# Performance work log

Measured on AMD Instinct MI355X. Metric: run time of the kernel, lower is better.

Reference implementation:

```python
import jax, jax.numpy as jnp
import numpy as np

N = 50000      # num nodes
E = 800000     # num edges
D = 128        # hidden_dim
H = 2          # num_heads
A = H * D      # all_head_size


def setup_inputs() -> dict:
    key = jax.random.key(0)
    ks = jax.random.split(key, 18)
    rn = lambda k, shape, s=1.0: jax.random.normal(k, shape, jnp.float32) * s
    w = 0.05  # small init scale for weights (glorot-ish)
    return {
        "x_0": rn(ks[0], (N, D)),
        "x_1": rn(ks[1], (N, D)),
        "edge_attr": rn(ks[2], (E, D)),
        "edges": jax.random.randint(ks[3], (2, E), 0, N, jnp.int64 if jax.config.jax_enable_x64 else jnp.int32),
        "edge_types": jax.random.randint(ks[4], (E,), 0, 8, jnp.int64 if jax.config.jax_enable_x64 else jnp.int32),
        # Attention projections (stored [in, out]; equals torch Linear y = x @ W)
        "Wq": rn(ks[5], (D, A), w),   "bq": jnp.zeros((A,), jnp.float32),
        "Wk": rn(ks[6], (2 * D, A), w), "bk": jnp.zeros((A,), jnp.float32),
        "Wv": rn(ks[7], (2 * D, A), w), "bv": jnp.zeros((A,), jnp.float32),
        "Wo": rn(ks[8], (A, D), w),   "bo": jnp.zeros((D,), jnp.float32),
        # GRUCell params: gates ordered (r, z, n) as in torch
        "W_ih": rn(ks[9], (D, 3 * D), w),  "b_ih": rn(ks[10], (3 * D,), w),
        "W_hh": rn(ks[11], (D, 3 * D), w), "b_hh": rn(ks[12], (3 * D,), w),
    }


def _gru_cell(x, h, W_ih, b_ih, W_hh, b_hh):
    gi = x @ W_ih + b_ih
    gh = h @ W_hh + b_hh
    i_r, i_z, i_n = jnp.split(gi, 3, axis=-1)
    h_r, h_z, h_n = jnp.split(gh, 3, axis=-1)
    r = jax.nn.sigmoid(i_r + h_r)
    z = jax.nn.sigmoid(i_z + h_z)
    n = jnp.tanh(i_n + r * h_n)
    return (1.0 - z) * n + z * h


def reference(x_0, x_1, edge_attr, edges, edge_types,
              Wq, bq, Wk, bk, Wv, bv, Wo, bo, W_ih, b_ih, W_hh, b_hh):
    src, dst = edges[0], edges[1]            # x_j <- src, x_i <- dst
    q = (x_0[dst] @ Wq + bq).reshape(-1, H, D)            # [E,H,D]
    kv_in = jnp.concatenate([edge_attr, x_1[src]], -1)    # [E,2D]
    k = (kv_in @ Wk + bk).reshape(-1, H, D)
    v = (kv_in @ Wv + bv).reshape(-1, H, D)
    alpha = jnp.sum(q * k, -1) / jnp.sqrt(jnp.float32(D)) # [E,H]
    alpha = jax.nn.leaky_relu(alpha, 0.2)
    # segment softmax over dst (PyG softmax semantics, eps = 1e-16)
    m = jax.ops.segment_max(alpha, dst, num_segments=N)
    e = jnp.exp(alpha - m[dst])
    denom = jax.ops.segment_sum(e, dst, num_segments=N)
    a = e / (denom[dst] + 1e-16)                           # [E,H]
    aggr = jax.ops.segment_sum(a[:, :, None] * v, dst, num_segments=N)  # [N,H,D]
    msg = aggr.reshape(N, A) @ Wo + bo                     # [N,D]
    # GRUCell(input=x_0, hidden=attn_message); target_idxes = all nodes
    return _gru_cell(x_0, msg, W_ih, b_ih, W_hh, b_hh)
```

## Files before the change

kernel.cpp:

```cpp
#include <hip/hip_runtime.h>
#include <hip/hip_bf16.h>
#include <math.h>

#define NN 50000
#define EE 800000
#define MPAD 50048

#define OFF_QQBF   0ull
#define OFF_KVBF   12900000ull
#define OFF_AGGBF  25900000ull
#define OFF_MSGBF  45300000ull
#define OFF_INT    48600000ull
#define OFF_WCATQ  50500000ull
#define OFF_WCATKV 50600000ull
#define OFF_WBIG   50700000ull
#define OFF_WGRU   50800000ull
#define OFF_BCATQ  51000000ull
#define OFF_BCATKV 51001000ull
#define OFF_BGRU   51002000ull
#define OFF_BO2    51003000ull
#define OFF_PQ     51010000ull
#define OFF_PKV    51050000ull
#define OFF_PBIG   51090000ull
#define OFF_PGRU   51130000ull
#define OFF_X0BF   51200000ull

typedef short bf16x8 __attribute__((ext_vector_type(8)));
typedef float f32x4 __attribute__((ext_vector_type(4)));
typedef float fv4 __attribute__((ext_vector_type(4)));

__device__ inline unsigned short f2bf(float f) {
  unsigned u = __float_as_uint(f);
  return (unsigned short)((u + 0x7FFFu + ((u >> 16) & 1u)) >> 16);
}
__device__ inline float bf2f(unsigned short u) {
  return __uint_as_float((unsigned)u << 16);
}
__device__ inline float4 bf2f4(ushort4 u) {
  float4 r;
  r.x = bf2f(u.x); r.y = bf2f(u.y); r.z = bf2f(u.z); r.w = bf2f(u.w);
  return r;
}

__global__ void prep_all(const float* __restrict__ Wq, const float* __restrict__ bq,
                         const float* __restrict__ Wk, const float* __restrict__ bk,
                         const float* __restrict__ Wv, const float* __restrict__ bv,
                         const float* __restrict__ Wo, const float* __restrict__ bo,
                         const float* __restrict__ W_ih, const float* __restrict__ b_ih,
                         const float* __restrict__ W_hh, const float* __restrict__ b_hh,
                         float* __restrict__ WcatQ, float* __restrict__ bcatQ,
                         float* __restrict__ WcatKV, float* __restrict__ bcatKV,
                         float* __restrict__ Wbig, float* __restrict__ WgruCat,
                         float* __restrict__ bgru, float* __restrict__ bo2,
                         int* __restrict__ zint) {
  const int bid = blockIdx.x, j = threadIdx.x;
  if (bid < 129) {
    int c0 = bid, h = j >> 7, c = j & 127;
    const float* wkrow = Wk + (size_t)c * 256 + h * 128;
    float acc = 0.f;
    if (c0 < 128) {
      const float* wqrow = Wq + (size_t)c0 * 256 + h * 128;
      for (int d = 0; d < 128; d++) acc += wqrow[d] * wkrow[d];
      WcatQ[c0 * 512 + 256 + j] = acc;
    } else {
      for (int d = 0; d < 128; d++) acc += bq[h * 128 + d] * wkrow[d];
      bcatQ[256 + j] = acc;
    }
  } else if (bid < 257) {
    int r = bid - 129;
    WcatQ[r * 512 + j] = Wq[r * 256 + j];
    if (j < 256) WcatKV[r * 256 + j] = Wk[(size_t)(128 + r) * 256 + j];
    if (r == 0) {
      bcatQ[j] = bq[j];
      if (j < 256) bcatKV[j] = bk[j];
    }
  } else if (bid < 513) {
    int r = (bid - 257) * 2 + (j >> 7), jj = j & 127;
    int h = (r >> 7) & 1, c = r & 127;
    int srow = (r < 256) ? c : 128 + c;
    float acc = 0.f;
    for (int d = 0; d < 128; d++)
      acc += Wv[(size_t)srow * 256 + h * 128 + d] * Wo[(size_t)(h * 128 + d) * 128 + jj];
    Wbig[r * 128 + jj] = acc;
  } else if (bid < 769) {
    int r = bid - 513;
    for (int c = j; c < 512; c += 256) {
      float v;
      if (r < 128) v = (c < 384) ? W_ih[(size_t)r * 384 + c] : 0.f;
      else {
        int rm = r - 128;
        v = (c < 256) ? W_hh[(size_t)rm * 384 + c]
                      : (c < 384 ? 0.f : W_hh[(size_t)rm * 384 + 256 + (c - 384)]);
      }
      WgruCat[(size_t)r * 512 + c] = v;
    }
  } else if (bid == 769) {
    bgru[j] = b_ih[j] + b_hh[j];
    int c1 = j + 256;
    bgru[c1] = (c1 < 384) ? b_ih[c1] : b_hh[c1 - 128];
  } else if (bid == 770) {
    if (j < 128) {
      float acc = bo[j];
      for (int t = 0; t < 256; t++) acc += bv[t] * Wo[(size_t)t * 128 + j];
      bo2[j] = acc;
    }
  } else {
    int g = ((bid - 771) * 256 + j) * 4;
    if (g < 2 * NN) *reinterpret_cast<int4*>(zint + g) = make_int4(0, 0, 0, 0);
  }
}

__global__ __launch_bounds__(1024) void pack_hist(
    const float* __restrict__ WcatQ, const float* __restrict__ WcatKV,
    const float* __restrict__ Wbig, const float* __restrict__ WgruCat,
    unsigned short* __restrict__ pQ, unsigned short* __restrict__ pKV,
    unsigned short* __restrict__ pBig, unsigned short* __restrict__ pGRU,
    const int* __restrict__ edges, int* __restrict__ cnt) {
  const int bid = blockIdx.x, tid = threadIdx.x;
  if (bid < 36) {
    int idx = bid * 1024 + tid;
    const float* W; unsigned short* P; int Nc;
    if (idx < 8192)       { W = WcatQ;   P = pQ;   Nc = 512; }
    else if (idx < 12288) { W = WcatKV;  P = pKV;  Nc = 256; idx -= 8192; }
    else if (idx < 20480) { W = Wbig;    P = pBig; Nc = 128; idx -= 12288; }
    else                  { W = WgruCat; P = pGRU; Nc = 512; idx -= 20480; }
    int nbs = Nc >> 4;
    int lane = idx & 63;
    int pair = idx >> 6;
    int kb = pair / nbs, nb = pair - kb * nbs;
    int kbase = kb * 32 + (lane >> 4) * 8;
    int col = nb * 16 + (lane & 15);
    unsigned short o[8];
#pragma unroll
    for (int j = 0; j < 8; ++j) o[j] = f2bf(W[(size_t)(kbase + j) * Nc + col]);
    *reinterpret_cast<bf16x8*>(P + (size_t)idx * 8) = *reinterpret_cast<bf16x8*>(o);
  } else {
    int e = (bid - 36) * 1024 + tid;
    if (e < EE) atomicAdd(&cnt[edges[EE + e]], 1);
  }
}

__global__ __launch_bounds__(1024) void scan_partial(const int* __restrict__ cnt,
                                                     int* __restrict__ basep,
                                                     int* __restrict__ bsum) {
  __shared__ int sd[1024];
  int t = threadIdx.x, g = blockIdx.x * 1024 + t;
  int v = (g < NN) ? cnt[g] : 0;
  sd[t] = v;
  __syncthreads();
  for (int d = 1; d < 1024; d <<= 1) {
    int add = (t >= d) ? sd[t - d] : 0;
    __syncthreads();
    sd[t] += add;
    __syncthreads();
  }
  if (g < NN) basep[g] = sd[t] - v;
  if (t == 1023) bsum[blockIdx.x] = sd[1023];
}

__global__ __launch_bounds__(1024) void scan_final(const int* __restrict__ bsum,
                                                   const int* __restrict__ basep,
                                                   int* __restrict__ base) {
  __shared__ int s_off;
  const int bid = blockIdx.x, tid = threadIdx.x;
  if (tid < 64) {
    int v = (tid < 49) ? bsum[tid] : 0;
    int incl = v;
#pragma unroll
    for (int off = 1; off < 64; off <<= 1) {
      int o = __shfl_up(incl, off);
      if (tid >= off) incl += o;
    }
    int ex = (bid == 0) ? 0 : __shfl(incl, bid - 1);
    if (tid == 0) s_off = ex;
  }
  __syncthreads();
  int g = bid * 1024 + tid;
  if (g < NN) base[g] = basep[g] + s_off;
  if (bid == 48 && tid == 0) base[NN] = EE;
}

template <int OUT, int AF32, int NF, int EMITA>
__device__ __forceinline__ void gemm_body(
    int bx, int by, const void* __restrict__ Av, const unsigned short* __restrict__ Wp,
    const float* __restrict__ bias, float* __restrict__ C,
    unsigned short* __restrict__ Cbf, unsigned short* __restrict__ Abf,
    int M, int Arows, int K, int Nc, int ldc) {
  const int wid = threadIdx.x >> 6, lane = threadIdx.x & 63;
  const int m0 = by * 64 + wid * 16;
  const int nb0 = bx * NF;
  const int nbs = Nc >> 4;
  const int row = m0 + (lane & 15);
  const int arow = min(row, Arows - 1);
  const int kq = lane >> 4;
  f32x4 acc[NF];
#pragma unroll
  for (int nf = 0; nf < NF; ++nf) acc[nf] = 0.f;
  const int nkb = K >> 5;
  for (int kb = 0; kb < nkb; ++kb) {
    bf16x8 a;
    if (AF32) {
      const float* ap = (const float*)Av + (size_t)arow * K + kb * 32 + kq * 8;
      const float4 f0 = *(const float4*)ap;
      const float4 f1 = *(const float4*)(ap + 4);
      unsigned short t[8] = {f2bf(f0.x), f2bf(f0.y), f2bf(f0.z), f2bf(f0.w),
                             f2bf(f1.x), f2bf(f1.y), f2bf(f1.z), f2bf(f1.w)};
      a = *reinterpret_cast<bf16x8*>(t);
      if (EMITA == 1) {
        if (bx == 0)
          *reinterpret_cast<bf16x8*>(Abf + (size_t)arow * K + kb * 32 + kq * 8) = a;
      } else if (EMITA == 2) {
        if (bx == 0)
          *reinterpret_cast<bf16x8*>(Abf + (size_t)arow * 384 + 256 +
                                     kb * 32 + kq * 8) = a;
      }
    } else {
      a = *reinterpret_cast<const bf16x8*>(
          (const unsigned short*)Av + (size_t)arow * K + kb * 32 + kq * 8);
    }
#pragma unroll
    for (int nf = 0; nf < NF; ++nf) {
      bf16x8 b = *reinterpret_cast<const bf16x8*>(
          Wp + ((size_t)(kb * nbs + nb0 + nf) * 64 + lane) * 8);
      acc[nf] = __builtin_amdgcn_mfma_f32_16x16x32_bf16(a, b, acc[nf], 0, 0, 0);
    }
  }
  const int crow0 = m0 + (lane >> 4) * 4;
  const int ccol = lane & 15;
#pragma unroll
  for (int nf = 0; nf < NF; ++nf) {
    const float bv = bias[(nb0 + nf) * 16 + ccol];
#pragma unroll
    for (int r = 0; r < 4; ++r) {
      float v = acc[nf][r] + bv;
      float vp = __shfl_xor(v, 1);
      const int rr = crow0 + r;
      if (rr < M) {
        if (OUT == 2)
          C[(size_t)rr * ldc + (nb0 + nf) * 16 + ccol] = v;
        if (!(lane & 1)) {
          ushort2 o;
          o.x = f2bf(v);
          o.y = f2bf(vp);
          *reinterpret_cast<ushort2*>(Cbf + (size_t)rr * ldc +
                                      (nb0 + nf) * 16 + (ccol & ~1)) = o;
        }
      }
    }
  }
}

template <int OUT, int AF32, int NF, int EMITA>
__global__ __launch_bounds__(256) void gemm_mfma(
    const void* __restrict__ Av, const unsigned short* __restrict__ Wp,
    const float* __restrict__ bias, float* __restrict__ C,
    unsigned short* __restrict__ Cbf, unsigned short* __restrict__ Abf,
    int M, int Arows, int K, int Nc, int ldc) {
  gemm_body<OUT, AF32, NF, EMITA>(blockIdx.x, blockIdx.y, Av, Wp, bias, C, Cbf,
                                  Abf, M, Arows, K, Nc, ldc);
}

__global__ __launch_bounds__(256) void scatter_proj(
    const int* __restrict__ edges, const int* __restrict__ base,
    int* __restrict__ cursor, int2* __restrict__ epairs,
    const float* __restrict__ x0, const float* __restrict__ x1,
    const unsigned short* __restrict__ pQ, const unsigned short* __restrict__ pKV,
    const float* __restrict__ bcatQ, const float* __restrict__ bcatKV,
    unsigned short* __restrict__ QQbf, unsigned short* __restrict__ KVbf,
    unsigned short* __restrict__ x0bf) {
  const int bid = blockIdx.x;
  if (bid < 3125) {
    int e = bid * 256 + threadIdx.x;
    int s = edges[e];
    int d = edges[EE + e];
    int pos = base[d] + atomicAdd(&cursor[d], 1);
    epairs[pos] = make_int2(e, s);
  } else if (bid < 6253) {
    int pb = bid - 3125;
    gemm_body<1, 1, 8, 1>(pb & 3, pb >> 2, x0, pQ, bcatQ, nullptr, QQbf, x0bf,
                          NN, NN, 128, 512, 512);
  } else {
    int pb = bid - 6253;
    gemm_body<1, 1, 8, 2>(pb & 1, pb >> 1, x1, pKV, bcatKV, nullptr, KVbf, KVbf,
                          NN, NN, 128, 256, 384);
  }
}

__global__ __launch_bounds__(256) void attn_wave_kernel(
    const float* __restrict__ edge_attr, const unsigned short* __restrict__ QQbf,
    const unsigned short* __restrict__ KVbf, const int* __restrict__ base,
    const int2* __restrict__ epairs, unsigned short* __restrict__ aggbf) {
  const int wid = threadIdx.x >> 6, lane = threadIdx.x & 63;
  const int n = blockIdx.x * 4 + wid;
  if (n >= NN) return;
  const int hh = lane >> 5;
  const int l = lane & 31;
  const unsigned short* qp = QQbf + (size_t)n * 512 + 4 * l;
  const float4 q0 = bf2f4(*(const ushort4*)(qp));
  const float4 q1 = bf2f4(*(const ushort4*)(qp + 128));
  const float4 w0 = bf2f4(*(const ushort4*)(qp + 256));
  const float4 w1 = bf2f4(*(const ushort4*)(qp + 384));
  const int beg = base[n], end = base[n + 1];
  float s0 = 0.f, s1 = 0.f;
  float4 ae0 = {0.f, 0.f, 0.f, 0.f}, ae1 = {0.f, 0.f, 0.f, 0.f};
  float4 av0 = {0.f, 0.f, 0.f, 0.f}, av1 = {0.f, 0.f, 0.f, 0.f};
  const float SC = 0.08838834764831845f;
  for (int p = beg; p < end; p += 2) {
    const int pe = min(p + hh, end - 1);
    const bool act = (p + hh < end);
    const int2 es = epairs[pe];
    const fv4 eav = __builtin_nontemporal_load(
        (const fv4*)(edge_attr + (size_t)es.x * 128 + 4 * l));
    const float4 ea = {eav.x, eav.y, eav.z, eav.w};
    const unsigned short* kp = KVbf + (size_t)es.y * 384 + 4 * l;
    const float4 k0 = bf2f4(*(const ushort4*)(kp));
    const float4 k1 = bf2f4(*(const ushort4*)(kp + 128));
    const float4 xb = bf2f4(*(const ushort4*)(kp + 256));
    float p0 = ea.x * w0.x + ea.y * w0.y + ea.z * w0.z + ea.w * w0.w
             + q0.x * k0.x + q0.y * k0.y + q0.z * k0.z + q0.w * k0.w;
    float p1 = ea.x * w1.x + ea.y * w1.y + ea.z * w1.z + ea.w * w1.w
             + q1.x * k1.x + q1.y * k1.y + q1.z * k1.z + q1.w * k1.w;
#pragma unroll
    for (int off = 16; off; off >>= 1) {
      p0 += __shfl_xor(p0, off);
      p1 += __shfl_xor(p1, off);
    }
    float a0 = p0 * SC; a0 = (a0 < 0.f) ? 0.2f * a0 : a0;
    float a1 = p1 * SC; a1 = (a1 < 0.f) ? 0.2f * a1 : a1;
    const float x0 = act ? __expf(a0) : 0.f;
    const float x1 = act ? __expf(a1) : 0.f;
    s0 += x0; s1 += x1;
    ae0.x += x0 * ea.x; ae0.y += x0 * ea.y; ae0.z += x0 * ea.z; ae0.w += x0 * ea.w;
    ae1.x += x1 * ea.x; ae1.y += x1 * ea.y; ae1.z += x1 * ea.z; ae1.w += x1 * ea.w;
    av0.x += x0 * xb.x; av0.y += x0 * xb.y; av0.z += x0 * xb.z; av0.w += x0 * xb.w;
    av1.x += x1 * xb.x; av1.y += x1 * xb.y; av1.z += x1 * xb.z; av1.w += x1 * xb.w;
  }
  s0 += __shfl_xor(s0, 32); s1 += __shfl_xor(s1, 32);
  ae0.x += __shfl_xor(ae0.x, 32); ae0.y += __shfl_xor(ae0.y, 32);
  ae0.z += __shfl_xor(ae0.z, 32); ae0.w += __shfl_xor(ae0.w, 32);
  ae1.x += __shfl_xor(ae1.x, 32); ae1.y += __shfl_xor(ae1.y, 32);
  ae1.z += __shfl_xor(ae1.z, 32); ae1.w += __shfl_xor(ae1.w, 32);
  av0.x += __shfl_xor(av0.x, 32); av0.y += __shfl_xor(av0.y, 32);
  av0.z += __shfl_xor(av0.z, 32); av0.w += __shfl_xor(av0.w, 32);
  av1.x += __shfl_xor(av1.x, 32); av1.y += __shfl_xor(av1.y, 32);
  av1.z += __shfl_xor(av1.z, 32); av1.w += __shfl_xor(av1.w, 32);
  const float i0 = 1.f / (s0 + 1e-16f), i1 = 1.f / (s1 + 1e-16f);
  if (hh == 0) {
    unsigned short* op = aggbf + (size_t)n * 512 + 4 * l;
    ushort4 o;
    o.x = f2bf(ae0.x * i0); o.y = f2bf(ae0.y * i0);
    o.z = f2bf(ae0.z * i0); o.w = f2bf(ae0.w * i0);
    *(ushort4*)op = o;
    o.x = f2bf(ae1.x * i1); o.y = f2bf(ae1.y * i1);
    o.z = f2bf(ae1.z * i1); o.w = f2bf(ae1.w * i1);
    *(ushort4*)(op + 128) = o;
    o.x = f2bf(av0.x * i0); o.y = f2bf(av0.y * i0);
    o.z = f2bf(av0.z * i0); o.w = f2bf(av0.w * i0);
    *(ushort4*)(op + 256) = o;
    o.x = f2bf(av1.x * i1); o.y = f2bf(av1.y * i1);
    o.z = f2bf(av1.z * i1); o.w = f2bf(av1.w * i1);
    *(ushort4*)(op + 384) = o;
  }
}

__global__ __launch_bounds__(256) void gru_fused(
    const unsigned short* __restrict__ x0bf, const unsigned short* __restrict__ msgbf,
    const unsigned short* __restrict__ pGRU, const float* __restrict__ bgru,
    float* __restrict__ out) {
  const int wid = threadIdx.x >> 6, lane = threadIdx.x & 63;
  const int m0 = blockIdx.y * 64 + wid * 16;
  const int xq = blockIdx.x;
  const int row = m0 + (lane & 15);
  const int ar = min(row, NN - 1);
  const int kq = lane >> 4;
  f32x4 acc[4][2];
#pragma unroll
  for (int g = 0; g < 4; ++g)
#pragma unroll
    for (int f = 0; f < 2; ++f) acc[g][f] = 0.f;
  for (int kb = 0; kb < 8; ++kb) {
    bf16x8 a;
    if (kb < 4) {
      a = *reinterpret_cast<const bf16x8*>(x0bf + (size_t)ar * 128 +
                                           kb * 32 + kq * 8);
    } else {
      a = *reinterpret_cast<const bf16x8*>(msgbf + (size_t)ar * 128 +
                                           (kb - 4) * 32 + kq * 8);
    }
#pragma unroll
    for (int g = 0; g < 4; ++g)
#pragma unroll
      for (int f = 0; f < 2; ++f) {
        const int nf = g * 8 + xq * 2 + f;
        bf16x8 b = *reinterpret_cast<const bf16x8*>(
            pGRU + ((size_t)(kb * 32 + nf) * 64 + lane) * 8);
        acc[g][f] = __builtin_amdgcn_mfma_f32_16x16x32_bf16(a, b, acc[g][f], 0, 0, 0);
      }
  }
  const int crow0 = m0 + (lane >> 4) * 4;
  const int ccol = lane & 15;
#pragma unroll
  for (int f = 0; f < 2; ++f) {
    const int d = xq * 32 + f * 16 + ccol;
    const float brs = bgru[d], bzs = bgru[128 + d];
    const float bin = bgru[256 + d], bhn = bgru[384 + d];
#pragma unroll
    for (int r = 0; r < 4; ++r) {
      const int rr = crow0 + r;
      if (rr < NN) {
        const float rs = acc[0][f][r] + brs;
        const float zs = acc[1][f][r] + bzs;
        const float iv = acc[2][f][r] + bin;
        const float hv = acc[3][f][r] + bhn;
        const float rg = 1.f / (1.f + __expf(-rs));
        const float zg = 1.f / (1.f + __expf(-zs));
        const float ng = tanhf(iv + rg * hv);
        const float h = bf2f(msgbf[(size_t)rr * 128 + d]);
        out[(size_t)rr * 128 + d] = (1.f - zg) * ng + zg * h;
      }
    }
  }
}

extern "C" void kernel_launch(void* const* d_in, const int* in_sizes, int n_in,
                              void* d_out, int out_size, void* d_ws, size_t ws_size,
                              hipStream_t stream) {
  const float* x0 = (const float*)d_in[0];
  const float* x1 = (const float*)d_in[1];
  const float* edge_attr = (const float*)d_in[2];
  const int* edges = (const int*)d_in[3];
  const float* Wq = (const float*)d_in[5];
  const float* bq = (const float*)d_in[6];
  const float* Wk = (const float*)d_in[7];
  const float* bk = (const float*)d_in[8];
  const float* Wv = (const float*)d_in[9];
  const float* bv = (const float*)d_in[10];
  const float* Wo = (const float*)d_in[11];
  const float* bo = (const float*)d_in[12];
  const float* W_ih = (const float*)d_in[13];
  const float* b_ih = (const float*)d_in[14];
  const float* W_hh = (const float*)d_in[15];
  const float* b_hh = (const float*)d_in[16];
  float* out = (float*)d_out;
  float* wsf = (float*)d_ws;

  unsigned short* QQbf  = (unsigned short*)(wsf + OFF_QQBF);
  unsigned short* KVbf  = (unsigned short*)(wsf + OFF_KVBF);
  unsigned short* aggbf = (unsigned short*)(wsf + OFF_AGGBF);
  unsigned short* msgbf = (unsigned short*)(wsf + OFF_MSGBF);
  unsigned short* x0bf  = (unsigned short*)(wsf + OFF_X0BF);
  int* ip    = (int*)(wsf + OFF_INT);
  int* cntb  = ip;
  int* curb  = ip + NN;
  int* bpart = ip + 2 * NN;
  int* baseb = ip + 3 * NN;
  int* bsumb = ip + 4 * NN + 1;
  int2* epairs = (int2*)(ip + 4 * NN + 130);
  float* WcatQ  = wsf + OFF_WCATQ;
  float* WcatKV = wsf + OFF_WCATKV;
  float* Wbigb  = wsf + OFF_WBIG;
  float* WgruC  = wsf + OFF_WGRU;
  float* bcatQ  = wsf + OFF_BCATQ;
  float* bcatKV = wsf + OFF_BCATKV;
  float* bgru   = wsf + OFF_BGRU;
  float* bo2    = wsf + OFF_BO2;
  unsigned short* pQ   = (unsigned short*)(wsf + OFF_PQ);
  unsigned short* pKV  = (unsigned short*)(wsf + OFF_PKV);
  unsigned short* pBig = (unsigned short*)(wsf + OFF_PBIG);
  unsigned short* pGRU = (unsigned short*)(wsf + OFF_PGRU);

  prep_all<<<871, 256, 0, stream>>>(Wq, bq, Wk, bk, Wv, bv, Wo, bo, W_ih, b_ih,
                                    W_hh, b_hh, WcatQ, bcatQ, WcatKV, bcatKV,
                                    Wbigb, WgruC, bgru, bo2, ip);
  pack_hist<<<818, 1024, 0, stream>>>(WcatQ, WcatKV, Wbigb, WgruC,
                                      pQ, pKV, pBig, pGRU, edges, cntb);
  scan_partial<<<49, 1024, 0, stream>>>(cntb, bpart, bsumb);
  scan_final<<<49, 1024, 0, stream>>>(bsumb, bpart, baseb);
  scatter_proj<<<7817, 256, 0, stream>>>(edges, baseb, curb, epairs,
                                         x0, x1, pQ, pKV, bcatQ, bcatKV,
                                         QQbf, KVbf, x0bf);
  attn_wave_kernel<<<(NN + 3) / 4, 256, 0, stream>>>(edge_attr, QQbf, KVbf,
                                                     baseb, epairs, aggbf);
  gemm_mfma<1, 0, 4, 0><<<dim3(2, MPAD / 64), 256, 0, stream>>>(
      aggbf, pBig, bo2, nullptr, msgbf, nullptr, NN, NN, 512, 128, 128);
  gru_fused<<<dim3(4, MPAD / 64), 256, 0, stream>>>(x0bf, msgbf, pGRU, bgru, out);
}
```

Measured before the change: 397.4 us.

## Fold Wk x1-part into per-node query weights, gather raw bf16 x1

```diff
diff --git a/kernel.cpp b/kernel.cpp
--- a/kernel.cpp
+++ b/kernel.cpp
@@ -7,23 +7,22 @@
 #define MPAD 50048
 
 #define OFF_QQBF   0ull
-#define OFF_KVBF   12900000ull
-#define OFF_AGGBF  25900000ull
-#define OFF_MSGBF  45300000ull
-#define OFF_INT    48600000ull
-#define OFF_WCATQ  50500000ull
-#define OFF_WCATKV 50600000ull
-#define OFF_WBIG   50700000ull
-#define OFF_WGRU   50800000ull
-#define OFF_BCATQ  51000000ull
-#define OFF_BCATKV 51001000ull
-#define OFF_BGRU   51002000ull
-#define OFF_BO2    51003000ull
-#define OFF_PQ     51010000ull
-#define OFF_PKV    51050000ull
-#define OFF_PBIG   51090000ull
-#define OFF_PGRU   51130000ull
-#define OFF_X0BF   51200000ull
+#define OFF_X1BF   12900000ull
+#define OFF_AGGBF  16200000ull
+#define OFF_MSGBF  29100000ull
+#define OFF_X0BF   32400000ull
+#define OFF_QB     35700000ull
+#define OFF_INT    35900000ull
+#define OFF_WCATQ  37800000ull
+#define OFF_WBIG   37900000ull
+#define OFF_WGRU   38000000ull
+#define OFF_BCATQ  38150000ull
+#define OFF_BGRU   38151000ull
+#define OFF_BO2    38152000ull
+#define OFF_WQB    38153000ull
+#define OFF_PQ     38160000ull
+#define OFF_PBIG   38200000ull
+#define OFF_PGRU   38240000ull
 
 typedef short bf16x8 __attribute__((ext_vector_type(8)));
 typedef float f32x4 __attribute__((ext_vector_type(4)));
@@ -49,41 +48,34 @@
                          const float* __restrict__ W_ih, const float* __restrict__ b_ih,
                          const float* __restrict__ W_hh, const float* __restrict__ b_hh,
                          float* __restrict__ WcatQ, float* __restrict__ bcatQ,
-                         float* __restrict__ WcatKV, float* __restrict__ bcatKV,
                          float* __restrict__ Wbig, float* __restrict__ WgruCat,
                          float* __restrict__ bgru, float* __restrict__ bo2,
-                         int* __restrict__ zint) {
+                         float* __restrict__ wqb, int* __restrict__ zint) {
   const int bid = blockIdx.x, j = threadIdx.x;
-  if (bid < 129) {
-    int c0 = bid, h = j >> 7, c = j & 127;
-    const float* wkrow = Wk + (size_t)c * 256 + h * 128;
+  if (bid < 258) {
+    int part = (bid < 129) ? 0 : 1;
+    int c0 = (part == 0) ? bid : bid - 129;
+    int h = j >> 7, c = j & 127;
+    const float* wkrow = Wk + (size_t)(part * 128 + c) * 256 + h * 128;
     float acc = 0.f;
     if (c0 < 128) {
       const float* wqrow = Wq + (size_t)c0 * 256 + h * 128;
       for (int d = 0; d < 128; d++) acc += wqrow[d] * wkrow[d];
-      WcatQ[c0 * 512 + 256 + j] = acc;
+      WcatQ[c0 * 512 + part * 256 + j] = acc;
     } else {
       for (int d = 0; d < 128; d++) acc += bq[h * 128 + d] * wkrow[d];
-      bcatQ[256 + j] = acc;
-    }
-  } else if (bid < 257) {
-    int r = bid - 129;
-    WcatQ[r * 512 + j] = Wq[r * 256 + j];
-    if (j < 256) WcatKV[r * 256 + j] = Wk[(size_t)(128 + r) * 256 + j];
-    if (r == 0) {
-      bcatQ[j] = bq[j];
-      if (j < 256) bcatKV[j] = bk[j];
-    }
-  } else if (bid < 513) {
-    int r = (bid - 257) * 2 + (j >> 7), jj = j & 127;
+      bcatQ[part * 256 + j] = acc;
+    }
+  } else if (bid < 514) {
+    int r = (bid - 258) * 2 + (j >> 7), jj = j & 127;
     int h = (r >> 7) & 1, c = r & 127;
     int srow = (r < 256) ? c : 128 + c;
     float acc = 0.f;
     for (int d = 0; d < 128; d++)
       acc += Wv[(size_t)srow * 256 + h * 128 + d] * Wo[(size_t)(h * 128 + d) * 128 + jj];
     Wbig[r * 128 + jj] = acc;
-  } else if (bid < 769) {
-    int r = bid - 513;
+  } else if (bid < 770) {
+    int r = bid - 514;
     for (int c = j; c < 512; c += 256) {
       float v;
       if (r < 128) v = (c < 384) ? W_ih[(size_t)r * 384 + c] : 0.f;
@@ -94,36 +86,45 @@
       }
       WgruCat[(size_t)r * 512 + c] = v;
     }
-  } else if (bid == 769) {
+  } else if (bid == 770) {
     bgru[j] = b_ih[j] + b_hh[j];
     int c1 = j + 256;
     bgru[c1] = (c1 < 384) ? b_ih[c1] : b_hh[c1 - 128];
-  } else if (bid == 770) {
+  } else if (bid == 771) {
+    int d = j >> 1, h = j & 1;
+    float acc = 0.f;
+    for (int t = 0; t < 128; t++) acc += Wq[(size_t)d * 256 + h * 128 + t] * bk[h * 128 + t];
+    wqb[j] = acc;
+    if (j < 2) {
+      float qc = 0.f;
+      for (int t = 0; t < 128; t++) qc += bq[j * 128 + t] * bk[j * 128 + t];
+      wqb[256 + j] = qc;
+    }
+  } else if (bid == 772) {
     if (j < 128) {
       float acc = bo[j];
       for (int t = 0; t < 256; t++) acc += bv[t] * Wo[(size_t)t * 128 + j];
       bo2[j] = acc;
     }
   } else {
-    int g = ((bid - 771) * 256 + j) * 4;
+    int g = ((bid - 773) * 256 + j) * 4;
     if (g < 2 * NN) *reinterpret_cast<int4*>(zint + g) = make_int4(0, 0, 0, 0);
   }
 }
 
 __global__ __launch_bounds__(1024) void pack_hist(
-    const float* __restrict__ WcatQ, const float* __restrict__ WcatKV,
-    const float* __restrict__ Wbig, const float* __restrict__ WgruCat,
-    unsigned short* __restrict__ pQ, unsigned short* __restrict__ pKV,
-    unsigned short* __restrict__ pBig, unsigned short* __restrict__ pGRU,
+    const float* __restrict__ WcatQ, const float* __restrict__ Wbig,
+    const float* __restrict__ WgruCat,
+    unsigned short* __restrict__ pQ, unsigned short* __restrict__ pBig,
+    unsigned short* __restrict__ pGRU,
     const int* __restrict__ edges, int* __restrict__ cnt) {
   const int bid = blockIdx.x, tid = threadIdx.x;
-  if (bid < 36) {
+  if (bid < 32) {
     int idx = bid * 1024 + tid;
     const float* W; unsigned short* P; int Nc;
     if (idx < 8192)       { W = WcatQ;   P = pQ;   Nc = 512; }
-    else if (idx < 12288) { W = WcatKV;  P = pKV;  Nc = 256; idx -= 8192; }
-    else if (idx < 20480) { W = Wbig;    P = pBig; Nc = 128; idx -= 12288; }
-    else                  { W = WgruCat; P = pGRU; Nc = 512; idx -= 20480; }
+    else if (idx < 16384) { W = Wbig;    P = pBig; Nc = 128; idx -= 8192; }
+    else                  { W = WgruCat; P = pGRU; Nc = 512; idx -= 16384; }
     int nbs = Nc >> 4;
     int lane = idx & 63;
     int pair = idx >> 6;
@@ -135,7 +136,7 @@
     for (int j = 0; j < 8; ++j) o[j] = f2bf(W[(size_t)(kbase + j) * Nc + col]);
     *reinterpret_cast<bf16x8*>(P + (size_t)idx * 8) = *reinterpret_cast<bf16x8*>(o);
   } else {
-    int e = (bid - 36) * 1024 + tid;
+    int e = (bid - 32) * 1024 + tid;
     if (e < EE) atomicAdd(&cnt[edges[EE + e]], 1);
   }
 }
@@ -206,13 +207,9 @@
       unsigned short t[8] = {f2bf(f0.x), f2bf(f0.y), f2bf(f0.z), f2bf(f0.w),
                              f2bf(f1.x), f2bf(f1.y), f2bf(f1.z), f2bf(f1.w)};
       a = *reinterpret_cast<bf16x8*>(t);
-      if (EMITA == 1) {
+      if (EMITA) {
         if (bx == 0)
           *reinterpret_cast<bf16x8*>(Abf + (size_t)arow * K + kb * 32 + kq * 8) = a;
-      } else if (EMITA == 2) {
-        if (bx == 0)
-          *reinterpret_cast<bf16x8*>(Abf + (size_t)arow * 384 + 256 +
-                                     kb * 32 + kq * 8) = a;
       }
     } else {
       a = *reinterpret_cast<const bf16x8*>(
@@ -264,13 +261,13 @@
     const int* __restrict__ edges, const int* __restrict__ base,
     int* __restrict__ cursor, int2* __restrict__ epairs,
     const float* __restrict__ x0, const float* __restrict__ x1,
-    const unsigned short* __restrict__ pQ, const unsigned short* __restrict__ pKV,
-    const float* __restrict__ bcatQ, const float* __restrict__ bcatKV,
-    unsigned short* __restrict__ QQbf, unsigned short* __restrict__ KVbf,
-    unsigned short* __restrict__ x0bf) {
-  const int bid = blockIdx.x;
+    const unsigned short* __restrict__ pQ, const float* __restrict__ bcatQ,
+    const float* __restrict__ wqb, unsigned short* __restrict__ QQbf,
+    unsigned short* __restrict__ x1bf, unsigned short* __restrict__ x0bf,
+    float* __restrict__ qb) {
+  const int bid = blockIdx.x, tid = threadIdx.x;
   if (bid < 3125) {
-    int e = bid * 256 + threadIdx.x;
+    int e = bid * 256 + tid;
     int s = edges[e];
     int d = edges[EE + e];
     int pos = base[d] + atomicAdd(&cursor[d], 1);
@@ -279,27 +276,55 @@
     int pb = bid - 3125;
     gemm_body<1, 1, 8, 1>(pb & 3, pb >> 2, x0, pQ, bcatQ, nullptr, QQbf, x0bf,
                           NN, NN, 128, 512, 512);
+  } else if (bid < 9381) {
+    int i = ((bid - 6253) * 256 + tid) * 8;
+    unsigned short o[8];
+    if (i + 8 <= NN * 128) {
+#pragma unroll
+      for (int j = 0; j < 8; ++j) o[j] = f2bf(x1[i + j]);
+    } else {
+#pragma unroll
+      for (int j = 0; j < 8; ++j) o[j] = (i + j < NN * 128) ? f2bf(x1[i + j]) : 0;
+    }
+    *reinterpret_cast<bf16x8*>(x1bf + i) = *reinterpret_cast<bf16x8*>(o);
   } else {
-    int pb = bid - 6253;
-    gemm_body<1, 1, 8, 2>(pb & 1, pb >> 1, x1, pKV, bcatKV, nullptr, KVbf, KVbf,
-                          NN, NN, 128, 256, 384);
+    int n = (bid - 9381) * 8 + (tid >> 5);
+    int l = tid & 31;
+    const fv4 x = *(const fv4*)(x0 + (size_t)n * 128 + 4 * l);
+    const fv4 wq0 = *(const fv4*)(wqb + 8 * l);
+    const fv4 wq1 = *(const fv4*)(wqb + 8 * l + 4);
+    float s0 = x.x * wq0.x + x.y * wq0.z + x.z * wq1.x + x.w * wq1.z;
+    float s1 = x.x * wq0.y + x.y * wq0.w + x.z * wq1.y + x.w * wq1.w;
+#pragma unroll
+    for (int off = 16; off; off >>= 1) {
+      s0 += __shfl_xor(s0, off);
+      s1 += __shfl_xor(s1, off);
+    }
+    if (l == 0) {
+      float2 o;
+      o.x = s0 + wqb[256];
+      o.y = s1 + wqb[257];
+      *(float2*)(qb + (size_t)n * 2) = o;
+    }
   }
 }
 
 __global__ __launch_bounds__(256) void attn_wave_kernel(
     const float* __restrict__ edge_attr, const unsigned short* __restrict__ QQbf,
-    const unsigned short* __restrict__ KVbf, const int* __restrict__ base,
-    const int2* __restrict__ epairs, unsigned short* __restrict__ aggbf) {
+    const unsigned short* __restrict__ x1bf, const float* __restrict__ qb,
+    const int* __restrict__ base, const int2* __restrict__ epairs,
+    unsigned short* __restrict__ aggbf) {
   const int wid = threadIdx.x >> 6, lane = threadIdx.x & 63;
   const int n = blockIdx.x * 4 + wid;
   if (n >= NN) return;
   const int hh = lane >> 5;
   const int l = lane & 31;
   const unsigned short* qp = QQbf + (size_t)n * 512 + 4 * l;
-  const float4 q0 = bf2f4(*(const ushort4*)(qp));
-  const float4 q1 = bf2f4(*(const ushort4*)(qp + 128));
-  const float4 w0 = bf2f4(*(const ushort4*)(qp + 256));
-  const float4 w1 = bf2f4(*(const ushort4*)(qp + 384));
+  const float4 w0 = bf2f4(*(const ushort4*)(qp));
+  const float4 w1 = bf2f4(*(const ushort4*)(qp + 128));
+  const float4 u0 = bf2f4(*(const ushort4*)(qp + 256));
+  const float4 u1 = bf2f4(*(const ushort4*)(qp + 384));
+  const float2 qbv = *(const float2*)(qb + (size_t)n * 2);
   const int beg = base[n], end = base[n + 1];
   float s0 = 0.f, s1 = 0.f;
   float4 ae0 = {0.f, 0.f, 0.f, 0.f}, ae1 = {0.f, 0.f, 0.f, 0.f};
@@ -312,21 +337,18 @@
     const fv4 eav = __builtin_nontemporal_load(
         (const fv4*)(edge_attr + (size_t)es.x * 128 + 4 * l));
     const float4 ea = {eav.x, eav.y, eav.z, eav.w};
-    const unsigned short* kp = KVbf + (size_t)es.y * 384 + 4 * l;
-    const float4 k0 = bf2f4(*(const ushort4*)(kp));
-    const float4 k1 = bf2f4(*(const ushort4*)(kp + 128));
-    const float4 xb = bf2f4(*(const ushort4*)(kp + 256));
+    const float4 xb = bf2f4(*(const ushort4*)(x1bf + (size_t)es.y * 128 + 4 * l));
     float p0 = ea.x * w0.x + ea.y * w0.y + ea.z * w0.z + ea.w * w0.w
-             + q0.x * k0.x + q0.y * k0.y + q0.z * k0.z + q0.w * k0.w;
+             + xb.x * u0.x + xb.y * u0.y + xb.z * u0.z + xb.w * u0.w;
     float p1 = ea.x * w1.x + ea.y * w1.y + ea.z * w1.z + ea.w * w1.w
-             + q1.x * k1.x + q1.y * k1.y + q1.z * k1.z + q1.w * k1.w;
+             + xb.x * u1.x + xb.y * u1.y + xb.z * u1.z + xb.w * u1.w;
 #pragma unroll
     for (int off = 16; off; off >>= 1) {
       p0 += __shfl_xor(p0, off);
       p1 += __shfl_xor(p1, off);
     }
-    float a0 = p0 * SC; a0 = (a0 < 0.f) ? 0.2f * a0 : a0;
-    float a1 = p1 * SC; a1 = (a1 < 0.f) ? 0.2f * a1 : a1;
+    float a0 = (p0 + qbv.x) * SC; a0 = (a0 < 0.f) ? 0.2f * a0 : a0;
+    float a1 = (p1 + qbv.y) * SC; a1 = (a1 < 0.f) ? 0.2f * a1 : a1;
     const float x0 = act ? __expf(a0) : 0.f;
     const float x1 = act ? __expf(a1) : 0.f;
     s0 += x0; s1 += x1;
@@ -445,10 +467,11 @@
   float* wsf = (float*)d_ws;
 
   unsigned short* QQbf  = (unsigned short*)(wsf + OFF_QQBF);
-  unsigned short* KVbf  = (unsigned short*)(wsf + OFF_KVBF);
+  unsigned short* x1bf  = (unsigned short*)(wsf + OFF_X1BF);
   unsigned short* aggbf = (unsigned short*)(wsf + OFF_AGGBF);
   unsigned short* msgbf = (unsigned short*)(wsf + OFF_MSGBF);
   unsigned short* x0bf  = (unsigned short*)(wsf + OFF_X0BF);
+  float* qb = wsf + OFF_QB;
   int* ip    = (int*)(wsf + OFF_INT);
   int* cntb  = ip;
   int* curb  = ip + NN;
@@ -457,29 +480,27 @@
   int* bsumb = ip + 4 * NN + 1;
   int2* epairs = (int2*)(ip + 4 * NN + 130);
   float* WcatQ  = wsf + OFF_WCATQ;
-  float* WcatKV = wsf + OFF_WCATKV;
   float* Wbigb  = wsf + OFF_WBIG;
   float* WgruC  = wsf + OFF_WGRU;
   float* bcatQ  = wsf + OFF_BCATQ;
-  float* bcatKV = wsf + OFF_BCATKV;
   float* bgru   = wsf + OFF_BGRU;
   float* bo2    = wsf + OFF_BO2;
+  float* wqb    = wsf + OFF_WQB;
   unsigned short* pQ   = (unsigned short*)(wsf + OFF_PQ);
-  unsigned short* pKV  = (unsigned short*)(wsf + OFF_PKV);
   unsigned short* pBig = (unsigned short*)(wsf + OFF_PBIG);
   unsigned short* pGRU = (unsigned short*)(wsf + OFF_PGRU);
 
-  prep_all<<<871, 256, 0, stream>>>(Wq, bq, Wk, bk, Wv, bv, Wo, bo, W_ih, b_ih,
-                                    W_hh, b_hh, WcatQ, bcatQ, WcatKV, bcatKV,
-                                    Wbigb, WgruC, bgru, bo2, ip);
-  pack_hist<<<818, 1024, 0, stream>>>(WcatQ, WcatKV, Wbigb, WgruC,
-                                      pQ, pKV, pBig, pGRU, edges, cntb);
+  prep_all<<<873, 256, 0, stream>>>(Wq, bq, Wk, bk, Wv, bv, Wo, bo, W_ih, b_ih,
+                                    W_hh, b_hh, WcatQ, bcatQ, Wbigb, WgruC,
+                                    bgru, bo2, wqb, ip);
+  pack_hist<<<814, 1024, 0, stream>>>(WcatQ, Wbigb, WgruC, pQ, pBig, pGRU,
+                                      edges, cntb);
   scan_partial<<<49, 1024, 0, stream>>>(cntb, bpart, bsumb);
   scan_final<<<49, 1024, 0, stream>>>(bsumb, bpart, baseb);
-  scatter_proj<<<7817, 256, 0, stream>>>(edges, baseb, curb, epairs,
-                                         x0, x1, pQ, pKV, bcatQ, bcatKV,
-                                         QQbf, KVbf, x0bf);
-  attn_wave_kernel<<<(NN + 3) / 4, 256, 0, stream>>>(edge_attr, QQbf, KVbf,
+  scatter_proj<<<15631, 256, 0, stream>>>(edges, baseb, curb, epairs,
+                                          x0, x1, pQ, bcatQ, wqb,
+                                          QQbf, x1bf, x0bf, qb);
+  attn_wave_kernel<<<(NN + 3) / 4, 256, 0, stream>>>(edge_attr, QQbf, x1bf, qb,
                                                      baseb, epairs, aggbf);
   gemm_mfma<1, 0, 4, 0><<<dim3(2, MPAD / 64), 256, 0, stream>>>(
       aggbf, pBig, bo2, nullptr, msgbf, nullptr, NN, NN, 512, 128, 128);
```

After: 379.5 us (median of 2 runs). -4.5%, faster.
